# Kernel tuning notes

Hardware: AMD Instinct MI355X
Metric: run time of the kernel (lower is better)

The kernel has to match this reference:

```python
import jax, jax.numpy as jnp
import numpy as np

# ---- HashGrid config (tcnn defaults from module __init__) ----
N_LEVELS = 6
F = 2                      # n_features_per_level
T = 2 ** 19                # hashmap size
BASE = 16                  # base_resolution, per_level_scale=2.0
_RES = [BASE * (2 ** l) for l in range(N_LEVELS)]          # 16..512
_SIZES = [min(r ** 3, T) for r in _RES]                    # dense if grid fits
_OFFSETS = [0] + list(np.cumsum(_SIZES))
TOTAL_ENTRIES = int(_OFFSETS[-1])
_PRIMES = (1, 2654435761, 805459861)
BOX_R = 1.0
DIM_H = 64
DIM_IN = 3 + N_LEVELS * F


def hash_encode(xn, grid):
    """Multi-res hash-grid encoding. xn: [N,3] in [0,1]; grid: [TOTAL_ENTRIES, F]."""
    feats = []
    for l in range(N_LEVELS):
        res, size, off = _RES[l], _SIZES[l], _OFFSETS[l]
        dense = (res ** 3) <= T
        pos = xn * jnp.float32(res - 1) + 0.5          # tcnn: scale*x + 0.5
        pg = jnp.floor(pos)
        frac = pos - pg                                # [N,3]
        pgi = pg.astype(jnp.uint32)
        acc = jnp.zeros((xn.shape[0], F), xn.dtype)
        for corner in range(8):                        # trilinear, 8 corners
            cb = jnp.array([(corner >> d) & 1 for d in range(3)], dtype=jnp.uint32)
            c = pgi + cb                               # [N,3] corner coords
            w = jnp.prod(jnp.where(cb == 1, frac, 1.0 - frac), axis=-1)  # [N]
            if dense:
                c = jnp.minimum(c, jnp.uint32(res - 1))
                idx = c[:, 0] + c[:, 1] * jnp.uint32(res) + c[:, 2] * jnp.uint32(res * res)
            else:
                idx = ((c[:, 0] * jnp.uint32(_PRIMES[0]))
                       ^ (c[:, 1] * jnp.uint32(_PRIMES[1]))
                       ^ (c[:, 2] * jnp.uint32(_PRIMES[2]))) % jnp.uint32(size)
            acc = acc + w[:, None] * grid[jnp.uint32(off) + idx]
        feats.append(acc)
    return jnp.concatenate(feats, axis=-1)             # [N, 12]


def setup_inputs() -> dict:
    key = jax.random.key(0)
    k0, k1, k2 = jax.random.split(key, 3)
    N = 2_097_152
    x = jax.random.uniform(k0, (N, 3), jnp.float32, -1.0, 1.0)
    grid = jax.random.uniform(k1, (TOTAL_ENTRIES, F), jnp.float32, -1e-2, 1e-2)
    W0 = jax.random.normal(k2, (DIM_IN, DIM_H), jnp.float32) * float(np.sqrt(2.0 / DIM_H))
    b0 = jnp.zeros((DIM_H,), jnp.float32)
    W1 = jnp.full((DIM_H, 1), float(np.sqrt(np.pi / DIM_H)), jnp.float32)
    b1 = jnp.full((1,), -1.0, jnp.float32)             # -init_radius
    return {"x": x, "grid": grid, "W0": W0, "b0": b0, "W1": W1, "b1": b1}


def reference(x, grid, W0, b0, W1, b1):
    xn = (x + BOX_R) / (2.0 * BOX_R)                   # normalize to [0,1]
    f = hash_encode(xn, grid)                          # [N,12]
    h = jnp.concatenate([x, f], axis=-1)               # [N,15]
    h = jax.nn.relu(h @ W0 + b0)                       # [N,64]
    return h @ W1 + b1                                 # [N,1] scalar level s
```

## Files before the change

kernel.cpp:

```cpp
#include <hip/hip_runtime.h>
#include <stdint.h>


typedef float vfloat2 __attribute__((ext_vector_type(2)));

static __device__ __forceinline__ unsigned umin_(unsigned a, unsigned b) {
    return a < b ? a : b;
}

#define HP1 2654435761u
#define HP2 805459861u
#define HMASK ((1u << 19) - 1u)

static __device__ __forceinline__ void gather8_sc0(
    const float2* __restrict__ tab, const unsigned* __restrict__ idx,
    vfloat2* __restrict__ v)
{
    uint64_t a0 = (uint64_t)(tab + idx[0]);
    uint64_t a1 = (uint64_t)(tab + idx[1]);
    uint64_t a2 = (uint64_t)(tab + idx[2]);
    uint64_t a3 = (uint64_t)(tab + idx[3]);
    uint64_t a4 = (uint64_t)(tab + idx[4]);
    uint64_t a5 = (uint64_t)(tab + idx[5]);
    uint64_t a6 = (uint64_t)(tab + idx[6]);
    uint64_t a7 = (uint64_t)(tab + idx[7]);
    asm volatile(
        "global_load_dwordx2 %0, %8, off sc0\n\t"
        "global_load_dwordx2 %1, %9, off sc0\n\t"
        "global_load_dwordx2 %2, %10, off sc0\n\t"
        "global_load_dwordx2 %3, %11, off sc0\n\t"
        "global_load_dwordx2 %4, %12, off sc0\n\t"
        "global_load_dwordx2 %5, %13, off sc0\n\t"
        "global_load_dwordx2 %6, %14, off sc0\n\t"
        "global_load_dwordx2 %7, %15, off sc0\n\t"
        "s_waitcnt vmcnt(0)"
        : "=&v"(v[0]), "=&v"(v[1]), "=&v"(v[2]), "=&v"(v[3]),
          "=&v"(v[4]), "=&v"(v[5]), "=&v"(v[6]), "=&v"(v[7])
        : "v"(a0), "v"(a1), "v"(a2), "v"(a3),
          "v"(a4), "v"(a5), "v"(a6), "v"(a7));
}

__global__ __launch_bounds__(256) void hash_level_kernel(
    const float* __restrict__ x,
    const float2* __restrict__ tab,
    float2* __restrict__ feat,
    float scale, int N)
{
    const int gid = blockIdx.x * 256 + threadIdx.x;
    if (gid >= N) return;

    const float px = __builtin_nontemporal_load(x + 3 * gid + 0);
    const float py = __builtin_nontemporal_load(x + 3 * gid + 1);
    const float pz = __builtin_nontemporal_load(x + 3 * gid + 2);

    const float p0 = fmaf((px + 1.0f) * 0.5f, scale, 0.5f);
    const float p1 = fmaf((py + 1.0f) * 0.5f, scale, 0.5f);
    const float p2 = fmaf((pz + 1.0f) * 0.5f, scale, 0.5f);
    const float g0 = floorf(p0), g1 = floorf(p1), g2 = floorf(p2);
    const float f0 = p0 - g0, f1 = p1 - g1, f2 = p2 - g2;
    const unsigned i0 = (unsigned)g0, i1 = (unsigned)g1, i2 = (unsigned)g2;

    const float wx[2] = {1.0f - f0, f0};
    const float wy[2] = {1.0f - f1, f1};
    const float wz[2] = {1.0f - f2, f2};
    const unsigned hx[2] = {i0, i0 + 1u};
    const unsigned hy[2] = {i1 * HP1, (i1 + 1u) * HP1};
    const unsigned hz[2] = {i2 * HP2, (i2 + 1u) * HP2};

    unsigned idx[8];
    float w[8];
    #pragma unroll
    for (int c = 0; c < 8; ++c) {
        const int bx = c & 1, by = (c >> 1) & 1, bz = (c >> 2) & 1;
        idx[c] = (hx[bx] ^ hy[by] ^ hz[bz]) & HMASK;
        w[c] = wx[bx] * wy[by] * wz[bz];
    }
    vfloat2 v[8];
    gather8_sc0(tab, idx, v);

    float a0 = 0.0f, a1 = 0.0f;
    #pragma unroll
    for (int c = 0; c < 8; ++c) {
        a0 = fmaf(w[c], v[c].x, a0);
        a1 = fmaf(w[c], v[c].y, a1);
    }
    float* fp = (float*)(feat + gid);
    __builtin_nontemporal_store(a0, fp + 0);
    __builtin_nontemporal_store(a1, fp + 1);
}

__global__ __launch_bounds__(256) void dense_mlp_kernel(
    const float* __restrict__ x,
    const float* __restrict__ grid,
    const float2* __restrict__ feat,
    const float* __restrict__ W0,
    const float* __restrict__ b0,
    const float* __restrict__ W1,
    const float* __restrict__ b1,
    float* __restrict__ out, int N)
{
    __shared__ float sW0T[64 * 16];
    __shared__ float sW1[64];

    const int tid = threadIdx.x;
    for (int t = tid; t < 960; t += 256) {
        int j = t / 15;
        int i = t - j * 15;
        sW0T[j * 16 + i] = W0[i * 64 + j];
    }
    if (tid < 64) {
        sW0T[tid * 16 + 15] = b0[tid];
        sW1[tid] = W1[tid];
    }
    __syncthreads();

    const int base = blockIdx.x * 1024 + tid;
    const float2* gtab = (const float2*)grid;

    float h[4][16];

    #pragma unroll
    for (int k = 0; k < 4; ++k) {
        const int g = base + 256 * k;
        const int gs = (g < N) ? g : 0;

        const float px = __builtin_nontemporal_load(x + 3 * gs + 0);
        const float py = __builtin_nontemporal_load(x + 3 * gs + 1);
        const float pz = __builtin_nontemporal_load(x + 3 * gs + 2);
        const float xn0 = (px + 1.0f) * 0.5f;
        const float xn1 = (py + 1.0f) * 0.5f;
        const float xn2 = (pz + 1.0f) * 0.5f;

        h[k][0] = px; h[k][1] = py; h[k][2] = pz;
        h[k][15] = 1.0f;

        constexpr int      RES01[2] = {16, 32};
        constexpr unsigned OFF01[2] = {0u, 4096u};
        #pragma unroll
        for (int l = 0; l < 2; ++l) {
            const float scale = (float)(RES01[l] - 1);
            const float p0 = fmaf(xn0, scale, 0.5f);
            const float p1 = fmaf(xn1, scale, 0.5f);
            const float p2 = fmaf(xn2, scale, 0.5f);
            const float g0 = floorf(p0), g1 = floorf(p1), g2 = floorf(p2);
            const float f0 = p0 - g0, f1 = p1 - g1, f2 = p2 - g2;
            const unsigned i0 = (unsigned)g0, i1 = (unsigned)g1, i2 = (unsigned)g2;

            const float wx[2] = {1.0f - f0, f0};
            const float wy[2] = {1.0f - f1, f1};
            const float wz[2] = {1.0f - f2, f2};
            const unsigned rm1 = (unsigned)(RES01[l] - 1);
            const unsigned res = (unsigned)RES01[l];
            const unsigned cx[2] = {umin_(i0, rm1), umin_(i0 + 1u, rm1)};
            const unsigned cy[2] = {umin_(i1, rm1) * res, umin_(i1 + 1u, rm1) * res};
            const unsigned cz[2] = {umin_(i2, rm1) * res * res,
                                    umin_(i2 + 1u, rm1) * res * res};
            float a0 = 0.0f, a1 = 0.0f;
            #pragma unroll
            for (int c = 0; c < 8; ++c) {
                const int bx = c & 1, by = (c >> 1) & 1, bz = (c >> 2) & 1;
                const unsigned idx = cx[bx] + cy[by] + cz[bz];
                const float ww = wx[bx] * wy[by] * wz[bz];
                const float2 v = gtab[OFF01[l] + idx];
                a0 = fmaf(ww, v.x, a0);
                a1 = fmaf(ww, v.y, a1);
            }
            h[k][3 + 2 * l] = a0;
            h[k][4 + 2 * l] = a1;
        }

        {
            const float p0 = fmaf(xn0, 63.0f, 0.5f);
            const float p1 = fmaf(xn1, 63.0f, 0.5f);
            const float p2 = fmaf(xn2, 63.0f, 0.5f);
            const float g0 = floorf(p0), g1 = floorf(p1), g2 = floorf(p2);
            const float f0 = p0 - g0, f1 = p1 - g1, f2 = p2 - g2;
            const unsigned i0 = (unsigned)g0, i1 = (unsigned)g1, i2 = (unsigned)g2;

            const float wx[2] = {1.0f - f0, f0};
            const float wy[2] = {1.0f - f1, f1};
            const float wz[2] = {1.0f - f2, f2};
            const unsigned cx[2] = {umin_(i0, 63u), umin_(i0 + 1u, 63u)};
            const unsigned cy[2] = {umin_(i1, 63u) * 64u, umin_(i1 + 1u, 63u) * 64u};
            const unsigned cz[2] = {umin_(i2, 63u) * 4096u, umin_(i2 + 1u, 63u) * 4096u};

            unsigned idx[8];
            float w[8];
            #pragma unroll
            for (int c = 0; c < 8; ++c) {
                const int bx = c & 1, by = (c >> 1) & 1, bz = (c >> 2) & 1;
                idx[c] = cx[bx] + cy[by] + cz[bz];
                w[c] = wx[bx] * wy[by] * wz[bz];
            }
            vfloat2 v[8];
            gather8_sc0(gtab + 36864u, idx, v);
            float a0 = 0.0f, a1 = 0.0f;
            #pragma unroll
            for (int c = 0; c < 8; ++c) {
                a0 = fmaf(w[c], v[c].x, a0);
                a1 = fmaf(w[c], v[c].y, a1);
            }
            h[k][7] = a0;
            h[k][8] = a1;
        }

        #pragma unroll
        for (int l = 0; l < 3; ++l) {
            const float* fp = (const float*)(feat + (size_t)l * N + gs);
            h[k][9 + 2 * l]  = __builtin_nontemporal_load(fp + 0);
            h[k][10 + 2 * l] = __builtin_nontemporal_load(fp + 1);
        }
    }

    const float b1v = b1[0];
    float o[4] = {b1v, b1v, b1v, b1v};

    #pragma unroll 2
    for (int j = 0; j < 64; ++j) {
        float4 wv[4];
        const float4* wrow = (const float4*)(sW0T + j * 16);
        wv[0] = wrow[0]; wv[1] = wrow[1]; wv[2] = wrow[2]; wv[3] = wrow[3];
        const float* wf = (const float*)wv;
        const float w1j = sW1[j];
        #pragma unroll
        for (int k = 0; k < 4; ++k) {
            float s = 0.0f;
            #pragma unroll
            for (int i = 0; i < 16; ++i)
                s = fmaf(h[k][i], wf[i], s);
            s = fmaxf(s, 0.0f);
            o[k] = fmaf(s, w1j, o[k]);
        }
    }

    #pragma unroll
    for (int k = 0; k < 4; ++k) {
        const int g = base + 256 * k;
        if (g < N) __builtin_nontemporal_store(o[k], out + g);
    }
}

extern "C" void kernel_launch(void* const* d_in, const int* in_sizes, int n_in,
                              void* d_out, int out_size, void* d_ws, size_t ws_size,
                              hipStream_t stream) {
    const float* x    = (const float*)d_in[0];
    const float* grid = (const float*)d_in[1];
    const float* W0   = (const float*)d_in[2];
    const float* b0   = (const float*)d_in[3];
    const float* W1   = (const float*)d_in[4];
    const float* b1   = (const float*)d_in[5];
    float* out = (float*)d_out;

    const int N = in_sizes[0] / 3;
    const int blocks1 = (N + 255) / 256;
    const int blocks4 = (N + 1023) / 1024;

    const float2* gtab = (const float2*)grid;
    float2* feat = (float2*)d_ws;

    hash_level_kernel<<<blocks1, 256, 0, stream>>>(x, gtab + 299008u,
                                                   feat + (size_t)0 * N, 127.0f, N);
    hash_level_kernel<<<blocks1, 256, 0, stream>>>(x, gtab + 823296u,
                                                   feat + (size_t)1 * N, 255.0f, N);
    hash_level_kernel<<<blocks1, 256, 0, stream>>>(x, gtab + 1347584u,
                                                   feat + (size_t)2 * N, 511.0f, N);
    dense_mlp_kernel<<<blocks4, 256, 0, stream>>>(x, grid, feat, W0, b0, W1, b1,
                                                  out, N);
}
```

Measured before the change: 375.1 us.

## Pair x-adjacent corners into single 16-byte loads when x index is even

When the integer x coordinate is even, the two x-neighbour corners (i0 and i0+1) sit in adjacent table entries: contiguous in the dense levels, and differing only in the lowest bit of the XOR hash index in the hashed levels. The kernels therefore fetch both with one aligned float4 load instead of two float2 loads, halving gather instructions for about half the points. The odd-x case keeps separate loads, and the inline-asm sc0 gather helper is dropped in favour of plain loads. The cost is a divergent branch inside each wavefront and loss of the explicit cache-policy bits.

After: 523.6 us. 39.6% more time.

```diff
diff --git a/kernel.cpp b/kernel.cpp
--- a/kernel.cpp
+++ b/kernel.cpp
@@ -1,43 +1,12 @@
 #include <hip/hip_runtime.h>
-#include <stdint.h>
-
-
-typedef float vfloat2 __attribute__((ext_vector_type(2)));
-
-static __device__ __forceinline__ unsigned umin_(unsigned a, unsigned b) {
-    return a < b ? a : b;
-}
+
 
 #define HP1 2654435761u
 #define HP2 805459861u
 #define HMASK ((1u << 19) - 1u)
 
-static __device__ __forceinline__ void gather8_sc0(
-    const float2* __restrict__ tab, const unsigned* __restrict__ idx,
-    vfloat2* __restrict__ v)
-{
-    uint64_t a0 = (uint64_t)(tab + idx[0]);
-    uint64_t a1 = (uint64_t)(tab + idx[1]);
-    uint64_t a2 = (uint64_t)(tab + idx[2]);
-    uint64_t a3 = (uint64_t)(tab + idx[3]);
-    uint64_t a4 = (uint64_t)(tab + idx[4]);
-    uint64_t a5 = (uint64_t)(tab + idx[5]);
-    uint64_t a6 = (uint64_t)(tab + idx[6]);
-    uint64_t a7 = (uint64_t)(tab + idx[7]);
-    asm volatile(
-        "global_load_dwordx2 %0, %8, off sc0\n\t"
-        "global_load_dwordx2 %1, %9, off sc0\n\t"
-        "global_load_dwordx2 %2, %10, off sc0\n\t"
-        "global_load_dwordx2 %3, %11, off sc0\n\t"
-        "global_load_dwordx2 %4, %12, off sc0\n\t"
-        "global_load_dwordx2 %5, %13, off sc0\n\t"
-        "global_load_dwordx2 %6, %14, off sc0\n\t"
-        "global_load_dwordx2 %7, %15, off sc0\n\t"
-        "s_waitcnt vmcnt(0)"
-        : "=&v"(v[0]), "=&v"(v[1]), "=&v"(v[2]), "=&v"(v[3]),
-          "=&v"(v[4]), "=&v"(v[5]), "=&v"(v[6]), "=&v"(v[7])
-        : "v"(a0), "v"(a1), "v"(a2), "v"(a3),
-          "v"(a4), "v"(a5), "v"(a6), "v"(a7));
+static __device__ __forceinline__ unsigned umin_(unsigned a, unsigned b) {
+    return a < b ? a : b;
 }
 
 __global__ __launch_bounds__(256) void hash_level_kernel(
@@ -60,33 +29,121 @@
     const float f0 = p0 - g0, f1 = p1 - g1, f2 = p2 - g2;
     const unsigned i0 = (unsigned)g0, i1 = (unsigned)g1, i2 = (unsigned)g2;
 
-    const float wx[2] = {1.0f - f0, f0};
     const float wy[2] = {1.0f - f1, f1};
     const float wz[2] = {1.0f - f2, f2};
-    const unsigned hx[2] = {i0, i0 + 1u};
     const unsigned hy[2] = {i1 * HP1, (i1 + 1u) * HP1};
     const unsigned hz[2] = {i2 * HP2, (i2 + 1u) * HP2};
 
-    unsigned idx[8];
-    float w[8];
-    #pragma unroll
-    for (int c = 0; c < 8; ++c) {
-        const int bx = c & 1, by = (c >> 1) & 1, bz = (c >> 2) & 1;
-        idx[c] = (hx[bx] ^ hy[by] ^ hz[bz]) & HMASK;
-        w[c] = wx[bx] * wy[by] * wz[bz];
-    }
-    vfloat2 v[8];
-    gather8_sc0(tab, idx, v);
-
-    float a0 = 0.0f, a1 = 0.0f;
-    #pragma unroll
-    for (int c = 0; c < 8; ++c) {
-        a0 = fmaf(w[c], v[c].x, a0);
-        a1 = fmaf(w[c], v[c].y, a1);
+    unsigned base[4];
+    float wyz[4];
+    #pragma unroll
+    for (int c = 0; c < 4; ++c) {
+        const int by = c & 1, bz = c >> 1;
+        base[c] = hy[by] ^ hz[bz];
+        wyz[c] = wy[by] * wz[bz];
+    }
+
+    float2 v0[4], v1[4];
+    if ((i0 & 1u) == 0u) {
+        float4 q[4];
+        #pragma unroll
+        for (int c = 0; c < 4; ++c) {
+            const unsigned pb = ((i0 ^ base[c]) & HMASK) & ~1u;
+            q[c] = *(const float4*)(tab + pb);
+        }
+        #pragma unroll
+        for (int c = 0; c < 4; ++c) {
+            const bool hi = (base[c] & 1u) != 0u;
+            const float2 lo2 = make_float2(q[c].x, q[c].y);
+            const float2 hi2 = make_float2(q[c].z, q[c].w);
+            v0[c] = hi ? hi2 : lo2;
+            v1[c] = hi ? lo2 : hi2;
+        }
+    } else {
+        unsigned a0[4], a1[4];
+        #pragma unroll
+        for (int c = 0; c < 4; ++c) {
+            a0[c] = (i0 ^ base[c]) & HMASK;
+            a1[c] = ((i0 + 1u) ^ base[c]) & HMASK;
+        }
+        #pragma unroll
+        for (int c = 0; c < 4; ++c) v0[c] = tab[a0[c]];
+        #pragma unroll
+        for (int c = 0; c < 4; ++c) v1[c] = tab[a1[c]];
+    }
+
+    const float wx0 = 1.0f - f0;
+    float acc0 = 0.0f, acc1 = 0.0f;
+    #pragma unroll
+    for (int c = 0; c < 4; ++c) {
+        const float wa = wx0 * wyz[c], wb = f0 * wyz[c];
+        acc0 = fmaf(wa, v0[c].x, acc0);
+        acc1 = fmaf(wa, v0[c].y, acc1);
+        acc0 = fmaf(wb, v1[c].x, acc0);
+        acc1 = fmaf(wb, v1[c].y, acc1);
     }
     float* fp = (float*)(feat + gid);
-    __builtin_nontemporal_store(a0, fp + 0);
-    __builtin_nontemporal_store(a1, fp + 1);
+    __builtin_nontemporal_store(acc0, fp + 0);
+    __builtin_nontemporal_store(acc1, fp + 1);
+}
+
+static __device__ __forceinline__ void dense_level(
+    const float2* __restrict__ tab, unsigned res,
+    float xn0, float xn1, float xn2, float& o0, float& o1)
+{
+    const float scale = (float)(res - 1);
+    const float p0 = fmaf(xn0, scale, 0.5f);
+    const float p1 = fmaf(xn1, scale, 0.5f);
+    const float p2 = fmaf(xn2, scale, 0.5f);
+    const float g0 = floorf(p0), g1 = floorf(p1), g2 = floorf(p2);
+    const float f0 = p0 - g0, f1 = p1 - g1, f2 = p2 - g2;
+    const unsigned i0 = (unsigned)g0, i1 = (unsigned)g1, i2 = (unsigned)g2;
+
+    const unsigned rm1 = res - 1u;
+    const unsigned cx0 = i0;
+    const unsigned cx1 = umin_(i0 + 1u, rm1);
+    const unsigned cy[2] = {umin_(i1, rm1) * res, umin_(i1 + 1u, rm1) * res};
+    const unsigned cz[2] = {umin_(i2, rm1) * res * res,
+                            umin_(i2 + 1u, rm1) * res * res};
+    const float wy[2] = {1.0f - f1, f1};
+    const float wz[2] = {1.0f - f2, f2};
+
+    unsigned yz[4];
+    float wyz[4];
+    #pragma unroll
+    for (int c = 0; c < 4; ++c) {
+        const int by = c & 1, bz = c >> 1;
+        yz[c] = cy[by] + cz[bz];
+        wyz[c] = wy[by] * wz[bz];
+    }
+
+    float2 v0[4], v1[4];
+    if ((i0 & 1u) == 0u) {
+        #pragma unroll
+        for (int c = 0; c < 4; ++c) {
+            const float4 q = *(const float4*)(tab + (cx0 + yz[c]));
+            v0[c] = make_float2(q.x, q.y);
+            v1[c] = make_float2(q.z, q.w);
+        }
+    } else {
+        #pragma unroll
+        for (int c = 0; c < 4; ++c) v0[c] = tab[cx0 + yz[c]];
+        #pragma unroll
+        for (int c = 0; c < 4; ++c) v1[c] = tab[cx1 + yz[c]];
+    }
+
+    const float wx0 = 1.0f - f0;
+    float acc0 = 0.0f, acc1 = 0.0f;
+    #pragma unroll
+    for (int c = 0; c < 4; ++c) {
+        const float wa = wx0 * wyz[c], wb = f0 * wyz[c];
+        acc0 = fmaf(wa, v0[c].x, acc0);
+        acc1 = fmaf(wa, v0[c].y, acc1);
+        acc0 = fmaf(wb, v1[c].x, acc0);
+        acc1 = fmaf(wb, v1[c].y, acc1);
+    }
+    o0 = acc0;
+    o1 = acc1;
 }
 
 __global__ __launch_bounds__(256) void dense_mlp_kernel(
@@ -134,75 +191,9 @@
         h[k][0] = px; h[k][1] = py; h[k][2] = pz;
         h[k][15] = 1.0f;
 
-        constexpr int      RES01[2] = {16, 32};
-        constexpr unsigned OFF01[2] = {0u, 4096u};
-        #pragma unroll
-        for (int l = 0; l < 2; ++l) {
-            const float scale = (float)(RES01[l] - 1);
-            const float p0 = fmaf(xn0, scale, 0.5f);
-            const float p1 = fmaf(xn1, scale, 0.5f);
-            const float p2 = fmaf(xn2, scale, 0.5f);
-            const float g0 = floorf(p0), g1 = floorf(p1), g2 = floorf(p2);
-            const float f0 = p0 - g0, f1 = p1 - g1, f2 = p2 - g2;
-            const unsigned i0 = (unsigned)g0, i1 = (unsigned)g1, i2 = (unsigned)g2;
-
-            const float wx[2] = {1.0f - f0, f0};
-            const float wy[2] = {1.0f - f1, f1};
-            const float wz[2] = {1.0f - f2, f2};
-            const unsigned rm1 = (unsigned)(RES01[l] - 1);
-            const unsigned res = (unsigned)RES01[l];
-            const unsigned cx[2] = {umin_(i0, rm1), umin_(i0 + 1u, rm1)};
-            const unsigned cy[2] = {umin_(i1, rm1) * res, umin_(i1 + 1u, rm1) * res};
-            const unsigned cz[2] = {umin_(i2, rm1) * res * res,
-                                    umin_(i2 + 1u, rm1) * res * res};
-            float a0 = 0.0f, a1 = 0.0f;
-            #pragma unroll
-            for (int c = 0; c < 8; ++c) {
-                const int bx = c & 1, by = (c >> 1) & 1, bz = (c >> 2) & 1;
-                const unsigned idx = cx[bx] + cy[by] + cz[bz];
-                const float ww = wx[bx] * wy[by] * wz[bz];
-                const float2 v = gtab[OFF01[l] + idx];
-                a0 = fmaf(ww, v.x, a0);
-                a1 = fmaf(ww, v.y, a1);
-            }
-            h[k][3 + 2 * l] = a0;
-            h[k][4 + 2 * l] = a1;
-        }
-
-        {
-            const float p0 = fmaf(xn0, 63.0f, 0.5f);
-            const float p1 = fmaf(xn1, 63.0f, 0.5f);
-            const float p2 = fmaf(xn2, 63.0f, 0.5f);
-            const float g0 = floorf(p0), g1 = floorf(p1), g2 = floorf(p2);
-            const float f0 = p0 - g0, f1 = p1 - g1, f2 = p2 - g2;
-            const unsigned i0 = (unsigned)g0, i1 = (unsigned)g1, i2 = (unsigned)g2;
-
-            const float wx[2] = {1.0f - f0, f0};
-            const float wy[2] = {1.0f - f1, f1};
-            const float wz[2] = {1.0f - f2, f2};
-            const unsigned cx[2] = {umin_(i0, 63u), umin_(i0 + 1u, 63u)};
-            const unsigned cy[2] = {umin_(i1, 63u) * 64u, umin_(i1 + 1u, 63u) * 64u};
-            const unsigned cz[2] = {umin_(i2, 63u) * 4096u, umin_(i2 + 1u, 63u) * 4096u};
-
-            unsigned idx[8];
-            float w[8];
-            #pragma unroll
-            for (int c = 0; c < 8; ++c) {
-                const int bx = c & 1, by = (c >> 1) & 1, bz = (c >> 2) & 1;
-                idx[c] = cx[bx] + cy[by] + cz[bz];
-                w[c] = wx[bx] * wy[by] * wz[bz];
-            }
-            vfloat2 v[8];
-            gather8_sc0(gtab + 36864u, idx, v);
-            float a0 = 0.0f, a1 = 0.0f;
-            #pragma unroll
-            for (int c = 0; c < 8; ++c) {
-                a0 = fmaf(w[c], v[c].x, a0);
-                a1 = fmaf(w[c], v[c].y, a1);
-            }
-            h[k][7] = a0;
-            h[k][8] = a1;
-        }
+        dense_level(gtab + 0u,     16u, xn0, xn1, xn2, h[k][3], h[k][4]);
+        dense_level(gtab + 4096u,  32u, xn0, xn1, xn2, h[k][5], h[k][6]);
+        dense_level(gtab + 36864u, 64u, xn0, xn1, xn2, h[k][7], h[k][8]);
 
         #pragma unroll
         for (int l = 0; l < 3; ++l) {
```
